# Optimization experiments

Hardware: AMD Instinct MI355X
Metric: run time of the kernel (lower is better)

Reference implementation:

```python
import jax, jax.numpy as jnp
import numpy as np

N = 100000
E = 1600000
F_IN = 128
HID = 64
N_CLASS = 40
NEG_SLOPE = 0.2


def setup_inputs() -> dict:
    key = jax.random.key(0)
    ks = jax.random.split(key, 16)
    s = lambda *sh: 1.0 / np.sqrt(sh[0])
    inp = {
        "x": jax.random.normal(ks[0], (N, F_IN), dtype=jnp.float32),
        "edge_index": jax.random.randint(ks[1], (2, E), 0, N, dtype=jnp.int64),
        "W1": jax.random.normal(ks[2], (F_IN, HID), jnp.float32) * s(F_IN),
        "b1": jnp.zeros((HID,), jnp.float32),
        "Wc0": jax.random.normal(ks[3], (HID, HID), jnp.float32) * s(HID),
        "att_src0": jax.random.normal(ks[4], (HID,), jnp.float32) * s(HID),
        "att_dst0": jax.random.normal(ks[5], (HID,), jnp.float32) * s(HID),
        "bias0": jnp.zeros((HID,), jnp.float32),
        "Wc1": jax.random.normal(ks[6], (HID, HID), jnp.float32) * s(HID),
        "att_src1": jax.random.normal(ks[7], (HID,), jnp.float32) * s(HID),
        "att_dst1": jax.random.normal(ks[8], (HID,), jnp.float32) * s(HID),
        "bias1": jnp.zeros((HID,), jnp.float32),
        "W2": jax.random.normal(ks[9], (HID, N_CLASS), jnp.float32) * s(HID),
        "b2": jnp.zeros((N_CLASS,), jnp.float32),
    }
    return inp


def gat_conv(x, src, dst, W, att_src, att_dst, bias):
    # x: [N, Fin]; src/dst: [E'] (self-loops already appended)
    h = x @ W                                   # [N, Fout]
    a_s = h @ att_src                           # [N]
    a_d = h @ att_dst                           # [N]
    e = jax.nn.leaky_relu(a_s[src] + a_d[dst], NEG_SLOPE)   # [E']
    # segment softmax over edges grouped by destination node
    e_max = jax.ops.segment_max(e, dst, num_segments=N)     # every node has a self-loop
    ex = jnp.exp(e - e_max[dst])
    denom = jax.ops.segment_sum(ex, dst, num_segments=N)
    alpha = ex / (denom[dst] + 1e-16)                        # [E']
    out = jax.ops.segment_sum(h[src] * alpha[:, None], dst, num_segments=N)
    return out + bias


def reference(x, edge_index, W1, b1, Wc0, att_src0, att_dst0, bias0,
              Wc1, att_src1, att_dst1, bias1, W2, b2):
    # eval mode: dropout_adj and feature dropout are identity
    loop = jnp.arange(N, dtype=edge_index.dtype)
    src = jnp.concatenate([edge_index[0], loop])
    dst = jnp.concatenate([edge_index[1], loop])

    h = jax.nn.relu(x @ W1 + b1)
    h = gat_conv(h, src, dst, Wc0, att_src0, att_dst0, bias0)
    h = jax.nn.relu(h)
    h = gat_conv(h, src, dst, Wc1, att_src1, att_dst1, bias1)
    logits = h @ W2 + b2
    return jax.nn.log_softmax(logits, axis=-1)
```

## Files before the change

### kernel.cpp

```cpp
#include <hip/hip_runtime.h>

#define N_NODES 100000
#define N_EDGES 1600000
#define F_IN    128
#define HID     64
#define N_CLASS 40
#define NEG_SLOPE 0.2f
#define ET (N_EDGES + N_NODES)
#define ROW_BLOCKS ((N_NODES + 63) / 64)

#define NCB   7
#define CAP1  294912
#define BPC   144
#define NFB   782
#define CAPF  2624
#define NT1   ((ET + 2047) / 2048)

typedef __attribute__((ext_vector_type(8))) short bf16x8;
typedef __attribute__((ext_vector_type(4))) float f32x4;

__device__ __forceinline__ unsigned int f2bf(float f) {
    unsigned int u = __float_as_uint(f);
    return (u + 0x7fffu + ((u >> 16) & 1u)) >> 16;
}

__global__ __launch_bounds__(256) void k_prepw(const float* __restrict__ W1,
        const float* __restrict__ Wc0, const float* __restrict__ Wc1,
        const float* __restrict__ W2,
        unsigned short* __restrict__ Wt1, unsigned short* __restrict__ Wtc0,
        unsigned short* __restrict__ Wtc1, unsigned short* __restrict__ W2t,
        int* __restrict__ zbuf, int zcount) {
    int g = blockIdx.x * 256 + threadIdx.x;
    int stride = gridDim.x * 256;
    for (int i = g; i < zcount; i += stride) zbuf[i] = 0;
    for (int i = g; i < F_IN * HID; i += stride) {
        int k = i >> 6, n = i & 63;
        Wt1[n * F_IN + k] = (unsigned short)f2bf(W1[i]);
    }
    for (int i = g; i < HID * HID; i += stride) {
        int k = i >> 6, n = i & 63;
        Wtc0[n * HID + k] = (unsigned short)f2bf(Wc0[i]);
        Wtc1[n * HID + k] = (unsigned short)f2bf(Wc1[i]);
    }
    for (int i = g; i < 48 * HID; i += stride) {
        int n = i >> 6, k = i & 63;
        W2t[n * HID + k] = (n < N_CLASS)
            ? (unsigned short)f2bf(W2[k * N_CLASS + n]) : (unsigned short)0;
    }
}

__global__ __launch_bounds__(256) void k_p1lin(
        const int* __restrict__ ei, int* __restrict__ tail1,
        unsigned int* __restrict__ buf1,
        const float* __restrict__ x, const unsigned short* __restrict__ Wt1,
        const float* __restrict__ b1, const unsigned short* __restrict__ Wtc0,
        const float* __restrict__ att_s, const float* __restrict__ att_d,
        unsigned short* __restrict__ hb, float* __restrict__ as_,
        float* __restrict__ ad_) {
    __shared__ __align__(16) char smem[17408];
    __shared__ int hist[NCB], lb[NCB], cbase[NCB];
    int t = threadIdx.x;
    int lane = t & 63, w = t >> 6;

    if (blockIdx.x < NT1) {
        unsigned int* eb = (unsigned int*)smem;
        int tileBase = blockIdx.x * 2048;
        int total = ET - tileBase; if (total > 2048) total = 2048;
        if (t < NCB) hist[t] = 0;
        __syncthreads();
        unsigned long long ltm = (1ull << lane) - 1ull;
        unsigned int pk[8]; int ps[8];
        #pragma unroll
        for (int r = 0; r < 8; ++r) {
            int i = tileBase + r * 256 + t;
            int s = 0, d = 0;
            bool valid = (i < ET);
            if (valid) {
                if (i < N_EDGES) { s = ei[i]; d = ei[N_EDGES + i]; }
                else             { s = d = i - N_EDGES; }
            }
            int b = valid ? (d >> 14) : -1;
            unsigned long long m[NCB];
            #pragma unroll
            for (int q = 0; q < NCB; ++q) m[q] = __ballot(b == q);
            int cnt = 0;
            #pragma unroll
            for (int q = 0; q < NCB; ++q) if (lane == q) cnt = __popcll(m[q]);
            int old = 0;
            if (lane < NCB) old = atomicAdd(&hist[lane], cnt);
            int bsafe = valid ? b : 0;
            int basew = __shfl(old, bsafe, 64);
            if (valid) {
                int rank = 0;
                #pragma unroll
                for (int q = 0; q < NCB; ++q)
                    if (b == q) rank = (int)__popcll(m[q] & ltm);
                pk[r] = ((unsigned int)s << 14) | ((unsigned int)d & 16383u);
                ps[r] = (basew + rank) | (b << 12);
            } else ps[r] = -1;
        }
        __syncthreads();
        if (t == 0) {
            int run = 0;
            #pragma unroll
            for (int q = 0; q < NCB; ++q) { int h = hist[q]; lb[q] = run; run += h; }
        }
        __syncthreads();
        if (t < NCB) {
            int g = (hist[t] > 0) ? atomicAdd(&tail1[t], hist[t]) : 0;
            cbase[t] = g - lb[t];
        }
        #pragma unroll
        for (int r = 0; r < 8; ++r) {
            if (ps[r] >= 0) {
                int b = ps[r] >> 12, pos = ps[r] & 4095;
                eb[lb[b] + pos] = pk[r];
            }
        }
        __syncthreads();
        int B1 = lb[1], B2 = lb[2], B3 = lb[3], B4 = lb[4], B5 = lb[5], B6 = lb[6];
        for (int j = t; j < total; j += 256) {
            unsigned int p = eb[j];
            int b = (j >= B1) + (j >= B2) + (j >= B3) + (j >= B4)
                  + (j >= B5) + (j >= B6);
            buf1[(size_t)b * CAP1 + cbase[b] + j] = p;
        }
    } else {
        int quad = lane >> 4, lr = lane & 15;
        int rowg0 = (int)(blockIdx.x - NT1) * 64 + w * 16;
        float* xs = (float*)smem + w * (16 * 68);

        int arow = rowg0 + lr; if (arow >= N_NODES) arow = N_NODES - 1;
        const float* ab = x + (size_t)arow * F_IN + quad * 8;
        float4 xa[8];
        #pragma unroll
        for (int kc = 0; kc < 4; ++kc) {
            xa[2 * kc]     = *(const float4*)(ab + kc * 32);
            xa[2 * kc + 1] = *(const float4*)(ab + kc * 32 + 4);
        }
        f32x4 zero = {0.f, 0.f, 0.f, 0.f};
        f32x4 acc[4] = {zero, zero, zero, zero};
        #pragma unroll
        for (int kc = 0; kc < 4; ++kc) {
            bf16x8 bw[4];
            #pragma unroll
            for (int nt = 0; nt < 4; ++nt)
                bw[nt] = *(const bf16x8*)(Wt1 + (nt * 16 + lr) * F_IN
                                          + kc * 32 + quad * 8);
            float4 a0 = xa[2 * kc], a1 = xa[2 * kc + 1];
            union { bf16x8 v; unsigned int u[4]; } af;
            af.u[0] = f2bf(a0.x) | (f2bf(a0.y) << 16);
            af.u[1] = f2bf(a0.z) | (f2bf(a0.w) << 16);
            af.u[2] = f2bf(a1.x) | (f2bf(a1.y) << 16);
            af.u[3] = f2bf(a1.z) | (f2bf(a1.w) << 16);
            #pragma unroll
            for (int nt = 0; nt < 4; ++nt)
                acc[nt] = __builtin_amdgcn_mfma_f32_16x16x32_bf16(
                              af.v, bw[nt], acc[nt], 0, 0, 0);
        }
        #pragma unroll
        for (int nt = 0; nt < 4; ++nt) {
            float bv = b1[nt * 16 + lr];
            #pragma unroll
            for (int reg = 0; reg < 4; ++reg)
                xs[(quad * 4 + reg) * 68 + nt * 16 + lr] =
                    fmaxf(acc[nt][reg] + bv, 0.f);
        }
        f32x4 acc2[4] = {zero, zero, zero, zero};
        #pragma unroll
        for (int kc = 0; kc < 2; ++kc) {
            bf16x8 bw[4];
            #pragma unroll
            for (int nt = 0; nt < 4; ++nt)
                bw[nt] = *(const bf16x8*)(Wtc0 + (nt * 16 + lr) * HID
                                          + kc * 32 + quad * 8);
            const float* ap = xs + lr * 68 + kc * 32 + quad * 8;
            float4 a0 = *(const float4*)ap;
            float4 a1 = *(const float4*)(ap + 4);
            union { bf16x8 v; unsigned int u[4]; } af;
            af.u[0] = f2bf(a0.x) | (f2bf(a0.y) << 16);
            af.u[1] = f2bf(a0.z) | (f2bf(a0.w) << 16);
            af.u[2] = f2bf(a1.x) | (f2bf(a1.y) << 16);
            af.u[3] = f2bf(a1.z) | (f2bf(a1.w) << 16);
            #pragma unroll
            for (int nt = 0; nt < 4; ++nt)
                acc2[nt] = __builtin_amdgcn_mfma_f32_16x16x32_bf16(
                              af.v, bw[nt], acc2[nt], 0, 0, 0);
        }
        float asv[4], adv[4];
        #pragma unroll
        for (int nt = 0; nt < 4; ++nt) {
            asv[nt] = att_s[nt * 16 + lr];
            adv[nt] = att_d[nt * 16 + lr];
        }
        #pragma unroll
        for (int reg = 0; reg < 4; ++reg) {
            float p1 = acc2[0][reg] * asv[0] + acc2[1][reg] * asv[1]
                     + acc2[2][reg] * asv[2] + acc2[3][reg] * asv[3];
            float p2 = acc2[0][reg] * adv[0] + acc2[1][reg] * adv[1]
                     + acc2[2][reg] * adv[2] + acc2[3][reg] * adv[3];
            #pragma unroll
            for (int off = 1; off < 16; off <<= 1) {
                p1 += __shfl_xor(p1, off, 64);
                p2 += __shfl_xor(p2, off, 64);
            }
            if (lr == 0) {
                int grow = rowg0 + quad * 4 + reg;
                if (grow < N_NODES) { as_[grow] = p1; ad_[grow] = p2; }
            }
        }
        #pragma unroll
        for (int nt = 0; nt < 4; ++nt)
            #pragma unroll
            for (int reg = 0; reg < 4; ++reg)
                xs[(quad * 4 + reg) * 68 + nt * 16 + lr] = acc2[nt][reg];
        #pragma unroll
        for (int j = 0; j < 2; ++j) {
            int task = j * 64 + lane;
            int r = task >> 3, g = task & 7;
            int grow = rowg0 + r;
            if (grow < N_NODES) {
                const float* p = xs + r * 68 + g * 8;
                uint4 u;
                u.x = f2bf(p[0]) | (f2bf(p[1]) << 16);
                u.y = f2bf(p[2]) | (f2bf(p[3]) << 16);
                u.z = f2bf(p[4]) | (f2bf(p[5]) << 16);
                u.w = f2bf(p[6]) | (f2bf(p[7]) << 16);
                *(uint4*)(hb + (size_t)grow * HID + g * 8) = u;
            }
        }
    }
}

__global__ __launch_bounds__(256) void k_part2(const unsigned int* __restrict__ buf1,
        const int* __restrict__ tail1, int* __restrict__ fcnt,
        unsigned int* __restrict__ buf2, int* __restrict__ fbase,
        int* __restrict__ rowptr, int* __restrict__ done0) {
    __shared__ unsigned int eb[2048];
    __shared__ int hist[128], lbase[128], loff[128], goff[128], sc[128];
    __shared__ int lastflag, wsum4[4];
    int t = threadIdx.x;
    int cb   = blockIdx.x / BPC;
    int tile = blockIdx.x % BPC;
    int n1 = tail1[cb];
    int base = tile * 2048;
    if (base < n1) {
        int total = n1 - base; if (total > 2048) total = 2048;
        if (t < 128) hist[t] = 0;
        __syncthreads();
        unsigned int pr[8]; int fr[8];
        #pragma unroll
        for (int r = 0; r < 8; ++r) {
            int i = base + r * 256 + t;
            int f = -1; unsigned int p = 0;
            if (i < n1) {
                p = buf1[(size_t)cb * CAP1 + i];
                f = (int)((p >> 7) & 127u);
                atomicAdd(&hist[f], 1);
            }
            pr[r] = p; fr[r] = f;
        }
        __syncthreads();
        if (t < 128) sc[t] = hist[t];
        __syncthreads();
        for (int off = 1; off < 128; off <<= 1) {
            int u = (t < 128 && t >= off) ? sc[t - off] : 0;
            __syncthreads();
            if (t < 128) sc[t] += u;
            __syncthreads();
        }
        if (t < 128) { lbase[t] = sc[t] - hist[t]; loff[t] = 0; }
        __syncthreads();
        if (t < 128 && hist[t] > 0)
            goff[t] = atomicAdd(&fcnt[cb * 128 + t], hist[t]);
        #pragma unroll
        for (int r = 0; r < 8; ++r) {
            if (fr[r] >= 0) {
                int f = fr[r];
                int pos = lbase[f] + atomicAdd(&loff[f], 1);
                eb[pos] = (pr[r] & 127u) | ((pr[r] >> 14) << 7)
                        | ((unsigned int)f << 24);
            }
        }
        __syncthreads();
        for (int j = t; j < total; j += 256) {
            unsigned int q = eb[j];
            int f = (int)(q >> 24);
            buf2[(size_t)(cb * 128 + f) * CAPF + goff[f] + (j - lbase[f])] =
                q & 0xFFFFFFu;
        }
    }
    if (t == 0) lastflag = (atomicAdd(done0, 1) == NCB * BPC - 1);
    __syncthreads();
    if (lastflag) {
        __threadfence();
        int k0 = t * 4;
        int v0 = (k0     < NFB) ? fcnt[k0]     : 0;
        int v1 = (k0 + 1 < NFB) ? fcnt[k0 + 1] : 0;
        int v2 = (k0 + 2 < NFB) ? fcnt[k0 + 2] : 0;
        int v3 = (k0 + 3 < NFB) ? fcnt[k0 + 3] : 0;
        int s1 = v0 + v1, s2 = s1 + v2, s3 = s2 + v3;
        int lane = t & 63, w = t >> 6;
        int ws = s3;
        #pragma unroll
        for (int off = 1; off < 64; off <<= 1) {
            int u = __shfl_up(ws, off, 64);
            if (lane >= off) ws += u;
        }
        if (lane == 63) wsum4[w] = ws;
        __syncthreads();
        int wb = 0;
        #pragma unroll
        for (int q = 0; q < 4; ++q) if (q < w) wb += wsum4[q];
        int ex = wb + ws - s3;
        if (k0     < NFB) fbase[k0]     = ex;
        if (k0 + 1 < NFB) fbase[k0 + 1] = ex + v0;
        if (k0 + 2 < NFB) fbase[k0 + 2] = ex + s1;
        if (k0 + 3 < NFB) fbase[k0 + 3] = ex + s2;
        if (t == 0) rowptr[N_NODES] = ET;
    }
}

__global__ __launch_bounds__(256) void k_part3(const unsigned int* __restrict__ buf2,
        const int* __restrict__ fcnt, const int* __restrict__ fbase,
        int* __restrict__ rowptr, int* __restrict__ col,
        int* __restrict__ dhistg, int* __restrict__ dbase,
        int* __restrict__ done1) {
    __shared__ unsigned int eb[CAPF];
    __shared__ int cs[CAPF];
    __shared__ int hist[128], lbase[128], loff[128], sc[128], dh[64];
    __shared__ int lastflag;
    int t = threadIdx.x;
    int fb = blockIdx.x;
    int nF = fcnt[fb];
    int gb = fbase[fb];
    int nbase = fb * 128;
    if (t < 128) hist[t] = 0;
    if (t >= 128 && t < 192) dh[t - 128] = 0;
    __syncthreads();
    for (int j = t; j < nF; j += 256) {
        unsigned int q = buf2[(size_t)fb * CAPF + j];
        eb[j] = q;
        atomicAdd(&hist[q & 127u], 1);
    }
    __syncthreads();
    if (t < 128) sc[t] = hist[t];
    __syncthreads();
    for (int off = 1; off < 128; off <<= 1) {
        int u = (t < 128 && t >= off) ? sc[t - off] : 0;
        __syncthreads();
        if (t < 128) sc[t] += u;
        __syncthreads();
    }
    if (t < 128) { lbase[t] = sc[t] - hist[t]; loff[t] = 0; }
    __syncthreads();
    if (t < 128 && nbase + t < N_NODES) {
        rowptr[nbase + t] = gb + lbase[t];
        int dg = hist[t]; if (dg > 63) dg = 63;
        atomicAdd(&dh[dg], 1);
    }
    for (int j = t; j < nF; j += 256) {
        unsigned int q = eb[j];
        int r = (int)(q & 127u);
        int p = lbase[r] + atomicAdd(&loff[r], 1);
        cs[p] = (int)(q >> 7);
    }
    __syncthreads();
    for (int j = t; j < nF; j += 256) col[gb + j] = cs[j];
    if (t < 64 && dh[t] > 0) atomicAdd(&dhistg[t], dh[t]);
    __syncthreads();
    if (t == 0) lastflag = (atomicAdd(done1, 1) == NFB - 1);
    __syncthreads();
    if (lastflag && t < 64) {
        __threadfence();
        int v = dhistg[t];
        int s = v;
        #pragma unroll
        for (int off = 1; off < 64; off <<= 1) {
            int u = __shfl_up(s, off, 64);
            if (t >= off) s += u;
        }
        dbase[t] = s - v;
    }
}

__global__ __launch_bounds__(256) void k_dscatter(const int* __restrict__ rowptr,
        int* __restrict__ dbase, int* __restrict__ nodeord) {
    __shared__ int lh[64], goff[64];
    int t = threadIdx.x;
    if (t < 64) lh[t] = 0;
    __syncthreads();
    int i = blockIdx.x * 256 + t;
    int deg = -1, lrank = 0;
    if (i < N_NODES) {
        deg = rowptr[i + 1] - rowptr[i];
        if (deg > 63) deg = 63;
        lrank = atomicAdd(&lh[deg], 1);
    }
    __syncthreads();
    if (t < 64) goff[t] = (lh[t] > 0) ? atomicAdd(&dbase[t], lh[t]) : 0;
    __syncthreads();
    if (deg >= 0) nodeord[goff[deg] + lrank] = i;
}

__global__ __launch_bounds__(256) void k_gemm_att(
        const unsigned short* __restrict__ hin,
        const unsigned short* __restrict__ Wt,
        const float* __restrict__ att_s, const float* __restrict__ att_d,
        unsigned short* __restrict__ hb, float* __restrict__ as_,
        float* __restrict__ ad_) {
    __shared__ float xs[4][16 * 68];
    int t = threadIdx.x;
    int lane = t & 63, w = t >> 6;
    int quad = lane >> 4, lr = lane & 15;
    int rowg0 = blockIdx.x * 64 + w * 16;

    bf16x8 bfr[2][4];
    #pragma unroll
    for (int kc = 0; kc < 2; ++kc)
        #pragma unroll
        for (int nt = 0; nt < 4; ++nt)
            bfr[kc][nt] = *(const bf16x8*)(Wt + (nt * 16 + lr) * HID
                                           + kc * 32 + quad * 8);
    f32x4 zero = {0.f, 0.f, 0.f, 0.f};
    f32x4 acc[4] = {zero, zero, zero, zero};

    int arow = rowg0 + lr; if (arow >= N_NODES) arow = N_NODES - 1;
    #pragma unroll
    for (int kc = 0; kc < 2; ++kc) {
        bf16x8 af = *(const bf16x8*)(hin + (size_t)arow * HID
                                     + kc * 32 + quad * 8);
        #pragma unroll
        for (int nt = 0; nt < 4; ++nt)
            acc[nt] = __builtin_amdgcn_mfma_f32_16x16x32_bf16(
                          af, bfr[kc][nt], acc[nt], 0, 0, 0);
    }
    float asv[4], adv[4];
    #pragma unroll
    for (int nt = 0; nt < 4; ++nt) {
        asv[nt] = att_s[nt * 16 + lr];
        adv[nt] = att_d[nt * 16 + lr];
    }
    #pragma unroll
    for (int reg = 0; reg < 4; ++reg) {
        float p1 = acc[0][reg] * asv[0] + acc[1][reg] * asv[1]
                 + acc[2][reg] * asv[2] + acc[3][reg] * asv[3];
        float p2 = acc[0][reg] * adv[0] + acc[1][reg] * adv[1]
                 + acc[2][reg] * adv[2] + acc[3][reg] * adv[3];
        #pragma unroll
        for (int off = 1; off < 16; off <<= 1) {
            p1 += __shfl_xor(p1, off, 64);
            p2 += __shfl_xor(p2, off, 64);
        }
        if (lr == 0) {
            int grow = rowg0 + quad * 4 + reg;
            if (grow < N_NODES) { as_[grow] = p1; ad_[grow] = p2; }
        }
    }
    #pragma unroll
    for (int nt = 0; nt < 4; ++nt)
        #pragma unroll
        for (int reg = 0; reg < 4; ++reg)
            xs[w][(quad * 4 + reg) * 68 + nt * 16 + lr] = acc[nt][reg];
    #pragma unroll
    for (int j = 0; j < 2; ++j) {
        int task = j * 64 + lane;
        int r = task >> 3, g = task & 7;
        int grow = rowg0 + r;
        if (grow < N_NODES) {
            const float* p = xs[w] + r * 68 + g * 8;
            uint4 u;
            u.x = f2bf(p[0]) | (f2bf(p[1]) << 16);
            u.y = f2bf(p[2]) | (f2bf(p[3]) << 16);
            u.z = f2bf(p[4]) | (f2bf(p[5]) << 16);
            u.w = f2bf(p[6]) | (f2bf(p[7]) << 16);
            *(uint4*)(hb + (size_t)grow * HID + g * 8) = u;
        }
    }
}

template <bool RELU>
__global__ __launch_bounds__(256) void k_gat_agg(const int* __restrict__ rowptr,
        const int* __restrict__ col, const unsigned short* __restrict__ hb,
        const float* __restrict__ as_, const float* __restrict__ ad_,
        const float* __restrict__ bias, const int* __restrict__ nodeord,
        unsigned short* __restrict__ outb) {
    int t = threadIdx.x;
    int lane = t & 63;
    int wid = blockIdx.x * 4 + (t >> 6);
    int l8 = lane & 7;
    int ch = l8 * 8;
    int d = nodeord[wid * 8 + (lane >> 3)];
    int beg = rowptr[d];
    int deg = rowptr[d + 1] - beg;
    float add = ad_[d];
    int degw = deg;
    degw = max(degw, __shfl_xor(degw, 8, 64));
    degw = max(degw, __shfl_xor(degw, 16, 64));
    degw = max(degw, __shfl_xor(degw, 32, 64));

    float a0=0.f,a1=0.f,a2=0.f,a3=0.f,a4=0.f,a5=0.f,a6=0.f,a7=0.f,den=0.f;
    const unsigned short* hch = hb + ch;
    for (int c = 0; c < degw; c += 8) {
        int idx = c + l8;
        int sj = 0; float wj = 0.f;
        if (idx < deg) {
            sj = col[beg + idx];
            float e = as_[sj] + add;
            e = (e > 0.f) ? e : NEG_SLOPE * e;
            wj = __expf(e);
        }
        uint4 hv[8]; float w0[8];
        #pragma unroll
        for (int j = 0; j < 8; ++j) {
            int sl = (lane & 56) | j;
            int s = __shfl(sj, sl, 64);
            w0[j] = __shfl(wj, sl, 64);
            hv[j] = *(const uint4*)(hch + (size_t)s * HID);
        }
        #pragma unroll
        for (int j = 0; j < 8; ++j) {
            den += w0[j];
            a0 = fmaf(w0[j], __uint_as_float(hv[j].x << 16),         a0);
            a1 = fmaf(w0[j], __uint_as_float(hv[j].x & 0xffff0000u), a1);
            a2 = fmaf(w0[j], __uint_as_float(hv[j].y << 16),         a2);
            a3 = fmaf(w0[j], __uint_as_float(hv[j].y & 0xffff0000u), a3);
            a4 = fmaf(w0[j], __uint_as_float(hv[j].z << 16),         a4);
            a5 = fmaf(w0[j], __uint_as_float(hv[j].z & 0xffff0000u), a5);
            a6 = fmaf(w0[j], __uint_as_float(hv[j].w << 16),         a6);
            a7 = fmaf(w0[j], __uint_as_float(hv[j].w & 0xffff0000u), a7);
        }
    }
    float inv = 1.f / (den + 1e-16f);
    float4 bA = *(const float4*)(bias + ch);
    float4 bB = *(const float4*)(bias + ch + 4);
    float o0 = fmaf(a0, inv, bA.x), o1 = fmaf(a1, inv, bA.y);
    float o2 = fmaf(a2, inv, bA.z), o3 = fmaf(a3, inv, bA.w);
    float o4 = fmaf(a4, inv, bB.x), o5 = fmaf(a5, inv, bB.y);
    float o6 = fmaf(a6, inv, bB.z), o7 = fmaf(a7, inv, bB.w);
    if (RELU) {
        o0 = fmaxf(o0, 0.f); o1 = fmaxf(o1, 0.f);
        o2 = fmaxf(o2, 0.f); o3 = fmaxf(o3, 0.f);
        o4 = fmaxf(o4, 0.f); o5 = fmaxf(o5, 0.f);
        o6 = fmaxf(o6, 0.f); o7 = fmaxf(o7, 0.f);
    }
    uint4 u;
    u.x = f2bf(o0) | (f2bf(o1) << 16);
    u.y = f2bf(o2) | (f2bf(o3) << 16);
    u.z = f2bf(o4) | (f2bf(o5) << 16);
    u.w = f2bf(o6) | (f2bf(o7) << 16);
    *(uint4*)(outb + (size_t)d * HID + ch) = u;
}

__global__ __launch_bounds__(256) void k_final(
        const unsigned short* __restrict__ aggb,
        const unsigned short* __restrict__ W2t, const float* __restrict__ b2,
        float* __restrict__ out) {
    __shared__ float xs[64 * 44];
    int t = threadIdx.x;
    int lane = t & 63, w = t >> 6;
    int quad = lane >> 4, lr = lane & 15;
    int rowg0 = blockIdx.x * 64 + w * 16;
    int base = blockIdx.x * 64;
    int rem = N_NODES - base; if (rem > 64) rem = 64;

    bf16x8 bfr[2][3];
    #pragma unroll
    for (int kc = 0; kc < 2; ++kc)
        #pragma unroll
        for (int nt = 0; nt < 3; ++nt)
            bfr[kc][nt] = *(const bf16x8*)(W2t + (nt * 16 + lr) * HID
                                           + kc * 32 + quad * 8);
    f32x4 zero = {0.f, 0.f, 0.f, 0.f};
    f32x4 acc[3] = {zero, zero, zero};
    int arow = rowg0 + lr; if (arow >= N_NODES) arow = N_NODES - 1;
    #pragma unroll
    for (int kc = 0; kc < 2; ++kc) {
        bf16x8 af = *(const bf16x8*)(aggb + (size_t)arow * HID
                                     + kc * 32 + quad * 8);
        #pragma unroll
        for (int nt = 0; nt < 3; ++nt)
            acc[nt] = __builtin_amdgcn_mfma_f32_16x16x32_bf16(
                          af, bfr[kc][nt], acc[nt], 0, 0, 0);
    }
    float bc[3];
    #pragma unroll
    for (int nt = 0; nt < 3; ++nt) {
        int cl = nt * 16 + lr;
        bc[nt] = (cl < N_CLASS) ? b2[cl] : -1e30f;
    }
    #pragma unroll
    for (int reg = 0; reg < 4; ++reg) {
        float v0 = acc[0][reg] + bc[0];
        float v1 = acc[1][reg] + bc[1];
        float v2 = acc[2][reg] + bc[2];
        float m = fmaxf(fmaxf(v0, v1), v2);
        #pragma unroll
        for (int off = 1; off < 16; off <<= 1)
            m = fmaxf(m, __shfl_xor(m, off, 64));
        float ss = __expf(v0 - m) + __expf(v1 - m) + __expf(v2 - m);
        #pragma unroll
        for (int off = 1; off < 16; off <<= 1)
            ss += __shfl_xor(ss, off, 64);
        float lse = m + logf(ss);
        int r = w * 16 + quad * 4 + reg;
        xs[r * 44 + lr]      = v0 - lse;
        xs[r * 44 + 16 + lr] = v1 - lse;
        if (lr < 8) xs[r * 44 + 32 + lr] = v2 - lse;
    }
    __syncthreads();
    #pragma unroll
    for (int j = 0; j < 3; ++j) {
        int idx = j * 256 + t;
        if (idx < rem * 10) {
            int r = idx / 10, c4 = idx - r * 10;
            float4 v = *(const float4*)(xs + r * 44 + c4 * 4);
            *(float4*)(out + (size_t)base * N_CLASS + idx * 4) = v;
        }
    }
}

extern "C" void kernel_launch(void* const* d_in, const int* in_sizes, int n_in,
                              void* d_out, int out_size, void* d_ws, size_t ws_size,
                              hipStream_t stream) {
    const float* x     = (const float*)d_in[0];
    const int*   ei    = (const int*)  d_in[1];
    const float* W1    = (const float*)d_in[2];
    const float* b1    = (const float*)d_in[3];
    const float* Wc0   = (const float*)d_in[4];
    const float* as0   = (const float*)d_in[5];
    const float* ad0   = (const float*)d_in[6];
    const float* bias0 = (const float*)d_in[7];
    const float* Wc1   = (const float*)d_in[8];
    const float* as1   = (const float*)d_in[9];
    const float* ad1   = (const float*)d_in[10];
    const float* bias1 = (const float*)d_in[11];
    const float* W2    = (const float*)d_in[12];
    const float* b2    = (const float*)d_in[13];
    float* out = (float*)d_out;

    char* p = (char*)d_ws;
    unsigned short* hb    = (unsigned short*)p; p += (size_t)N_NODES * HID * 2;
    unsigned short* agg0b = (unsigned short*)p; p += (size_t)N_NODES * HID * 2;
    char* pbuf = p;
    unsigned int*   buf1  = (unsigned int*)pbuf;
    unsigned int*   buf2  = (unsigned int*)(pbuf + (size_t)NCB * CAP1 * 4);
    unsigned short* agg1b = (unsigned short*)pbuf;
    p += (size_t)NCB * CAP1 * 4 + (size_t)NFB * CAPF * 4;
    int* col = (int*)p;                          p += (size_t)ET * 4;
    unsigned short* Wt1  = (unsigned short*)p;   p += F_IN * HID * 2;
    unsigned short* Wtc0 = (unsigned short*)p;   p += HID * HID * 2;
    unsigned short* Wtc1 = (unsigned short*)p;   p += HID * HID * 2;
    unsigned short* W2t  = (unsigned short*)p;   p += 48 * HID * 2;
    float* as_ = (float*)p;                      p += (size_t)N_NODES * 4;
    float* ad_ = (float*)p;                      p += (size_t)N_NODES * 4;
    int* tail1 = (int*)p;
    int* fcnt  = tail1 + NCB;
    int* fbase = fcnt + NFB;
    int* dhist = fbase + NFB;
    int* dbase = dhist + 64;
    int* done  = dbase + 64;
    const int ZCOUNT = NCB + 2 * NFB + 128 + 2;
    p += (size_t)ZCOUNT * 4;
    int* rowptr  = (int*)p;                      p += (size_t)(N_NODES + 1) * 4;
    int* nodeord = (int*)p;

    const int AGG_BLOCKS  = N_NODES / 32;
    const int NODE_BLOCKS = (N_NODES + 255) / 256;

    k_prepw<<<32, 256, 0, stream>>>(W1, Wc0, Wc1, W2, Wt1, Wtc0, Wtc1, W2t,
                                    tail1, ZCOUNT);
    k_p1lin<<<NT1 + ROW_BLOCKS, 256, 0, stream>>>(
        ei, tail1, buf1, x, Wt1, b1, Wtc0, as0, ad0, hb, as_, ad_);
    k_part2<<<NCB * BPC, 256, 0, stream>>>(buf1, tail1, fcnt, buf2, fbase,
                                           rowptr, done + 0);
    k_part3<<<NFB, 256, 0, stream>>>(buf2, fcnt, fbase, rowptr, col, dhist,
                                     dbase, done + 1);
    k_dscatter<<<NODE_BLOCKS, 256, 0, stream>>>(rowptr, dbase, nodeord);

    k_gat_agg<true><<<AGG_BLOCKS, 256, 0, stream>>>(
        rowptr, col, hb, as_, ad_, bias0, nodeord, agg0b);

    k_gemm_att<<<ROW_BLOCKS, 256, 0, stream>>>(agg0b, Wtc1, as1, ad1,
                                               hb, as_, ad_);
    k_gat_agg<false><<<AGG_BLOCKS, 256, 0, stream>>>(
        rowptr, col, hb, as_, ad_, bias1, nodeord, agg1b);

    k_final<<<ROW_BLOCKS, 256, 0, stream>>>(agg1b, W2t, b2, out);
}
```

Before: 289.9 us.

## Fuse next-layer linear and final classifier into GAT aggregation kernels

Removes the separate gemm_att and final classifier kernels. Each node's aggregated row is staged in LDS and multiplied by Wc1 (layer 0) or W2 with log-softmax (layer 1) inside the aggregation kernel, using fp32 FMAs instead of MFMA. It also software-pipelines the col/attention-weight fetch one chunk ahead in the aggregation loop and pads the degree histogram counters to separate cache lines. This saves two launches and a round trip of intermediates through memory, at the cost of scalar per-lane GEMM work, global weight reads in the inner loop, and uncoalesced 5-float output stores.

```diff
diff --git a/kernel.cpp b/kernel.cpp
--- a/kernel.cpp
+++ b/kernel.cpp
@@ -25,10 +25,8 @@
 }
 
 __global__ __launch_bounds__(256) void k_prepw(const float* __restrict__ W1,
-        const float* __restrict__ Wc0, const float* __restrict__ Wc1,
-        const float* __restrict__ W2,
+        const float* __restrict__ Wc0,
         unsigned short* __restrict__ Wt1, unsigned short* __restrict__ Wtc0,
-        unsigned short* __restrict__ Wtc1, unsigned short* __restrict__ W2t,
         int* __restrict__ zbuf, int zcount) {
     int g = blockIdx.x * 256 + threadIdx.x;
     int stride = gridDim.x * 256;
@@ -40,12 +38,6 @@
     for (int i = g; i < HID * HID; i += stride) {
         int k = i >> 6, n = i & 63;
         Wtc0[n * HID + k] = (unsigned short)f2bf(Wc0[i]);
-        Wtc1[n * HID + k] = (unsigned short)f2bf(Wc1[i]);
-    }
-    for (int i = g; i < 48 * HID; i += stride) {
-        int n = i >> 6, k = i & 63;
-        W2t[n * HID + k] = (n < N_CLASS)
-            ? (unsigned short)f2bf(W2[k * N_CLASS + n]) : (unsigned short)0;
     }
 }
 
@@ -367,20 +359,20 @@
     }
     __syncthreads();
     for (int j = t; j < nF; j += 256) col[gb + j] = cs[j];
-    if (t < 64 && dh[t] > 0) atomicAdd(&dhistg[t], dh[t]);
+    if (t < 64 && dh[t] > 0) atomicAdd(&dhistg[t * 16], dh[t]);
     __syncthreads();
     if (t == 0) lastflag = (atomicAdd(done1, 1) == NFB - 1);
     __syncthreads();
     if (lastflag && t < 64) {
         __threadfence();
-        int v = dhistg[t];
+        int v = dhistg[t * 16];
         int s = v;
         #pragma unroll
         for (int off = 1; off < 64; off <<= 1) {
             int u = __shfl_up(s, off, 64);
             if (t >= off) s += u;
         }
-        dbase[t] = s - v;
+        dbase[t * 16] = s - v;
     }
 }
 
@@ -398,99 +390,31 @@
         lrank = atomicAdd(&lh[deg], 1);
     }
     __syncthreads();
-    if (t < 64) goff[t] = (lh[t] > 0) ? atomicAdd(&dbase[t], lh[t]) : 0;
+    if (t < 64) goff[t] = (lh[t] > 0) ? atomicAdd(&dbase[t * 16], lh[t]) : 0;
     __syncthreads();
     if (deg >= 0) nodeord[goff[deg] + lrank] = i;
 }
 
-__global__ __launch_bounds__(256) void k_gemm_att(
-        const unsigned short* __restrict__ hin,
-        const unsigned short* __restrict__ Wt,
-        const float* __restrict__ att_s, const float* __restrict__ att_d,
-        unsigned short* __restrict__ hb, float* __restrict__ as_,
-        float* __restrict__ ad_) {
-    __shared__ float xs[4][16 * 68];
-    int t = threadIdx.x;
-    int lane = t & 63, w = t >> 6;
-    int quad = lane >> 4, lr = lane & 15;
-    int rowg0 = blockIdx.x * 64 + w * 16;
-
-    bf16x8 bfr[2][4];
-    #pragma unroll
-    for (int kc = 0; kc < 2; ++kc)
-        #pragma unroll
-        for (int nt = 0; nt < 4; ++nt)
-            bfr[kc][nt] = *(const bf16x8*)(Wt + (nt * 16 + lr) * HID
-                                           + kc * 32 + quad * 8);
-    f32x4 zero = {0.f, 0.f, 0.f, 0.f};
-    f32x4 acc[4] = {zero, zero, zero, zero};
-
-    int arow = rowg0 + lr; if (arow >= N_NODES) arow = N_NODES - 1;
-    #pragma unroll
-    for (int kc = 0; kc < 2; ++kc) {
-        bf16x8 af = *(const bf16x8*)(hin + (size_t)arow * HID
-                                     + kc * 32 + quad * 8);
-        #pragma unroll
-        for (int nt = 0; nt < 4; ++nt)
-            acc[nt] = __builtin_amdgcn_mfma_f32_16x16x32_bf16(
-                          af, bfr[kc][nt], acc[nt], 0, 0, 0);
-    }
-    float asv[4], adv[4];
-    #pragma unroll
-    for (int nt = 0; nt < 4; ++nt) {
-        asv[nt] = att_s[nt * 16 + lr];
-        adv[nt] = att_d[nt * 16 + lr];
-    }
-    #pragma unroll
-    for (int reg = 0; reg < 4; ++reg) {
-        float p1 = acc[0][reg] * asv[0] + acc[1][reg] * asv[1]
-                 + acc[2][reg] * asv[2] + acc[3][reg] * asv[3];
-        float p2 = acc[0][reg] * adv[0] + acc[1][reg] * adv[1]
-                 + acc[2][reg] * adv[2] + acc[3][reg] * adv[3];
-        #pragma unroll
-        for (int off = 1; off < 16; off <<= 1) {
-            p1 += __shfl_xor(p1, off, 64);
-            p2 += __shfl_xor(p2, off, 64);
-        }
-        if (lr == 0) {
-            int grow = rowg0 + quad * 4 + reg;
-            if (grow < N_NODES) { as_[grow] = p1; ad_[grow] = p2; }
-        }
-    }
-    #pragma unroll
-    for (int nt = 0; nt < 4; ++nt)
-        #pragma unroll
-        for (int reg = 0; reg < 4; ++reg)
-            xs[w][(quad * 4 + reg) * 68 + nt * 16 + lr] = acc[nt][reg];
-    #pragma unroll
-    for (int j = 0; j < 2; ++j) {
-        int task = j * 64 + lane;
-        int r = task >> 3, g = task & 7;
-        int grow = rowg0 + r;
-        if (grow < N_NODES) {
-            const float* p = xs[w] + r * 68 + g * 8;
-            uint4 u;
-            u.x = f2bf(p[0]) | (f2bf(p[1]) << 16);
-            u.y = f2bf(p[2]) | (f2bf(p[3]) << 16);
-            u.z = f2bf(p[4]) | (f2bf(p[5]) << 16);
-            u.w = f2bf(p[6]) | (f2bf(p[7]) << 16);
-            *(uint4*)(hb + (size_t)grow * HID + g * 8) = u;
-        }
-    }
-}
-
-template <bool RELU>
-__global__ __launch_bounds__(256) void k_gat_agg(const int* __restrict__ rowptr,
-        const int* __restrict__ col, const unsigned short* __restrict__ hb,
+template <int LAYER>
+__global__ __launch_bounds__(256) void k_agg(const int* __restrict__ rowptr,
+        const int* __restrict__ col, const unsigned short* __restrict__ hin,
         const float* __restrict__ as_, const float* __restrict__ ad_,
         const float* __restrict__ bias, const int* __restrict__ nodeord,
-        unsigned short* __restrict__ outb) {
+        const float* __restrict__ Wn,
+        const float* __restrict__ attS, const float* __restrict__ attD,
+        const float* __restrict__ b2,
+        unsigned short* __restrict__ hout,
+        float* __restrict__ aso, float* __restrict__ ado,
+        float* __restrict__ out) {
+    __shared__ float rows[4][8][68];
     int t = threadIdx.x;
     int lane = t & 63;
-    int wid = blockIdx.x * 4 + (t >> 6);
+    int w = t >> 6;
+    int wid = blockIdx.x * 4 + w;
     int l8 = lane & 7;
+    int g = lane >> 3;
     int ch = l8 * 8;
-    int d = nodeord[wid * 8 + (lane >> 3)];
+    int d = nodeord[wid * 8 + g];
     int beg = rowptr[d];
     int deg = rowptr[d + 1] - beg;
     float add = ad_[d];
@@ -500,16 +424,16 @@
     degw = max(degw, __shfl_xor(degw, 32, 64));
 
     float a0=0.f,a1=0.f,a2=0.f,a3=0.f,a4=0.f,a5=0.f,a6=0.f,a7=0.f,den=0.f;
-    const unsigned short* hch = hb + ch;
+    const unsigned short* hch = hin + ch;
+
+    int sj = 0; float wj = 0.f;
+    if (l8 < deg) {
+        sj = col[beg + l8];
+        float e = as_[sj] + add;
+        e = (e > 0.f) ? e : NEG_SLOPE * e;
+        wj = __expf(e);
+    }
     for (int c = 0; c < degw; c += 8) {
-        int idx = c + l8;
-        int sj = 0; float wj = 0.f;
-        if (idx < deg) {
-            sj = col[beg + idx];
-            float e = as_[sj] + add;
-            e = (e > 0.f) ? e : NEG_SLOPE * e;
-            wj = __expf(e);
-        }
         uint4 hv[8]; float w0[8];
         #pragma unroll
         for (int j = 0; j < 8; ++j) {
@@ -518,6 +442,15 @@
             w0[j] = __shfl(wj, sl, 64);
             hv[j] = *(const uint4*)(hch + (size_t)s * HID);
         }
+        int sjn = 0; float wjn = 0.f;
+        int idxn = c + 8 + l8;
+        if (c + 8 < degw && idxn < deg) {
+            sjn = col[beg + idxn];
+            float e = as_[sjn] + add;
+            e = (e > 0.f) ? e : NEG_SLOPE * e;
+            wjn = __expf(e);
+        }
+        __builtin_amdgcn_sched_barrier(0);
         #pragma unroll
         for (int j = 0; j < 8; ++j) {
             den += w0[j];
@@ -530,6 +463,7 @@
             a6 = fmaf(w0[j], __uint_as_float(hv[j].w << 16),         a6);
             a7 = fmaf(w0[j], __uint_as_float(hv[j].w & 0xffff0000u), a7);
         }
+        sj = sjn; wj = wjn;
     }
     float inv = 1.f / (den + 1e-16f);
     float4 bA = *(const float4*)(bias + ch);
@@ -538,85 +472,84 @@
     float o2 = fmaf(a2, inv, bA.z), o3 = fmaf(a3, inv, bA.w);
     float o4 = fmaf(a4, inv, bB.x), o5 = fmaf(a5, inv, bB.y);
     float o6 = fmaf(a6, inv, bB.z), o7 = fmaf(a7, inv, bB.w);
-    if (RELU) {
+    if (LAYER == 0) {
         o0 = fmaxf(o0, 0.f); o1 = fmaxf(o1, 0.f);
         o2 = fmaxf(o2, 0.f); o3 = fmaxf(o3, 0.f);
         o4 = fmaxf(o4, 0.f); o5 = fmaxf(o5, 0.f);
         o6 = fmaxf(o6, 0.f); o7 = fmaxf(o7, 0.f);
     }
-    uint4 u;
-    u.x = f2bf(o0) | (f2bf(o1) << 16);
-    u.y = f2bf(o2) | (f2bf(o3) << 16);
-    u.z = f2bf(o4) | (f2bf(o5) << 16);
-    u.w = f2bf(o6) | (f2bf(o7) << 16);
-    *(uint4*)(outb + (size_t)d * HID + ch) = u;
-}
-
-__global__ __launch_bounds__(256) void k_final(
-        const unsigned short* __restrict__ aggb,
-        const unsigned short* __restrict__ W2t, const float* __restrict__ b2,
-        float* __restrict__ out) {
-    __shared__ float xs[64 * 44];
-    int t = threadIdx.x;
-    int lane = t & 63, w = t >> 6;
-    int quad = lane >> 4, lr = lane & 15;
-    int rowg0 = blockIdx.x * 64 + w * 16;
-    int base = blockIdx.x * 64;
-    int rem = N_NODES - base; if (rem > 64) rem = 64;
-
-    bf16x8 bfr[2][3];
-    #pragma unroll
-    for (int kc = 0; kc < 2; ++kc)
-        #pragma unroll
-        for (int nt = 0; nt < 3; ++nt)
-            bfr[kc][nt] = *(const bf16x8*)(W2t + (nt * 16 + lr) * HID
-                                           + kc * 32 + quad * 8);
-    f32x4 zero = {0.f, 0.f, 0.f, 0.f};
-    f32x4 acc[3] = {zero, zero, zero};
-    int arow = rowg0 + lr; if (arow >= N_NODES) arow = N_NODES - 1;
-    #pragma unroll
-    for (int kc = 0; kc < 2; ++kc) {
-        bf16x8 af = *(const bf16x8*)(aggb + (size_t)arow * HID
-                                     + kc * 32 + quad * 8);
-        #pragma unroll
-        for (int nt = 0; nt < 3; ++nt)
-            acc[nt] = __builtin_amdgcn_mfma_f32_16x16x32_bf16(
-                          af, bfr[kc][nt], acc[nt], 0, 0, 0);
-    }
-    float bc[3];
-    #pragma unroll
-    for (int nt = 0; nt < 3; ++nt) {
-        int cl = nt * 16 + lr;
-        bc[nt] = (cl < N_CLASS) ? b2[cl] : -1e30f;
-    }
-    #pragma unroll
-    for (int reg = 0; reg < 4; ++reg) {
-        float v0 = acc[0][reg] + bc[0];
-        float v1 = acc[1][reg] + bc[1];
-        float v2 = acc[2][reg] + bc[2];
-        float m = fmaxf(fmaxf(v0, v1), v2);
-        #pragma unroll
-        for (int off = 1; off < 16; off <<= 1)
-            m = fmaxf(m, __shfl_xor(m, off, 64));
-        float ss = __expf(v0 - m) + __expf(v1 - m) + __expf(v2 - m);
-        #pragma unroll
-        for (int off = 1; off < 16; off <<= 1)
-            ss += __shfl_xor(ss, off, 64);
+
+    float* myrow = &rows[w][g][0];
+    myrow[ch + 0] = o0; myrow[ch + 1] = o1; myrow[ch + 2] = o2;
+    myrow[ch + 3] = o3; myrow[ch + 4] = o4; myrow[ch + 5] = o5;
+    myrow[ch + 6] = o6; myrow[ch + 7] = o7;
+
+    if (LAYER == 0) {
+        float h1[8] = {0,0,0,0,0,0,0,0};
+        for (int k = 0; k < 64; k += 4) {
+            float4 rv = *(const float4*)(myrow + k);
+            #pragma unroll
+            for (int kk = 0; kk < 4; ++kk) {
+                float r = (kk == 0) ? rv.x : (kk == 1) ? rv.y
+                        : (kk == 2) ? rv.z : rv.w;
+                float4 wa = *(const float4*)(Wn + (k + kk) * 64 + ch);
+                float4 wb = *(const float4*)(Wn + (k + kk) * 64 + ch + 4);
+                h1[0] = fmaf(r, wa.x, h1[0]); h1[1] = fmaf(r, wa.y, h1[1]);
+                h1[2] = fmaf(r, wa.z, h1[2]); h1[3] = fmaf(r, wa.w, h1[3]);
+                h1[4] = fmaf(r, wb.x, h1[4]); h1[5] = fmaf(r, wb.y, h1[5]);
+                h1[6] = fmaf(r, wb.z, h1[6]); h1[7] = fmaf(r, wb.w, h1[7]);
+            }
+        }
+        float4 sA = *(const float4*)(attS + ch);
+        float4 sB = *(const float4*)(attS + ch + 4);
+        float4 dA = *(const float4*)(attD + ch);
+        float4 dB = *(const float4*)(attD + ch + 4);
+        float p1 = h1[0]*sA.x + h1[1]*sA.y + h1[2]*sA.z + h1[3]*sA.w
+                 + h1[4]*sB.x + h1[5]*sB.y + h1[6]*sB.z + h1[7]*sB.w;
+        float p2 = h1[0]*dA.x + h1[1]*dA.y + h1[2]*dA.z + h1[3]*dA.w
+                 + h1[4]*dB.x + h1[5]*dB.y + h1[6]*dB.z + h1[7]*dB.w;
+        p1 += __shfl_xor(p1, 1, 64); p1 += __shfl_xor(p1, 2, 64);
+        p1 += __shfl_xor(p1, 4, 64);
+        p2 += __shfl_xor(p2, 1, 64); p2 += __shfl_xor(p2, 2, 64);
+        p2 += __shfl_xor(p2, 4, 64);
+        if (l8 == 0) { aso[d] = p1; ado[d] = p2; }
+        uint4 u;
+        u.x = f2bf(h1[0]) | (f2bf(h1[1]) << 16);
+        u.y = f2bf(h1[2]) | (f2bf(h1[3]) << 16);
+        u.z = f2bf(h1[4]) | (f2bf(h1[5]) << 16);
+        u.w = f2bf(h1[6]) | (f2bf(h1[7]) << 16);
+        *(uint4*)(hout + (size_t)d * HID + ch) = u;
+    } else {
+        int nb = l8 * 5;
+        float lg[5];
+        #pragma unroll
+        for (int c = 0; c < 5; ++c) lg[c] = b2[nb + c];
+        for (int k = 0; k < 64; k += 4) {
+            float4 rv = *(const float4*)(myrow + k);
+            #pragma unroll
+            for (int kk = 0; kk < 4; ++kk) {
+                float r = (kk == 0) ? rv.x : (kk == 1) ? rv.y
+                        : (kk == 2) ? rv.z : rv.w;
+                const float* wr = Wn + (k + kk) * N_CLASS + nb;
+                lg[0] = fmaf(r, wr[0], lg[0]);
+                lg[1] = fmaf(r, wr[1], lg[1]);
+                lg[2] = fmaf(r, wr[2], lg[2]);
+                lg[3] = fmaf(r, wr[3], lg[3]);
+                lg[4] = fmaf(r, wr[4], lg[4]);
+            }
+        }
+        float m = fmaxf(fmaxf(fmaxf(lg[0], lg[1]), fmaxf(lg[2], lg[3])), lg[4]);
+        m = fmaxf(m, __shfl_xor(m, 1, 64));
+        m = fmaxf(m, __shfl_xor(m, 2, 64));
+        m = fmaxf(m, __shfl_xor(m, 4, 64));
+        float ss = __expf(lg[0]-m) + __expf(lg[1]-m) + __expf(lg[2]-m)
+                 + __expf(lg[3]-m) + __expf(lg[4]-m);
+        ss += __shfl_xor(ss, 1, 64); ss += __shfl_xor(ss, 2, 64);
+        ss += __shfl_xor(ss, 4, 64);
         float lse = m + logf(ss);
-        int r = w * 16 + quad * 4 + reg;
-        xs[r * 44 + lr]      = v0 - lse;
-        xs[r * 44 + 16 + lr] = v1 - lse;
-        if (lr < 8) xs[r * 44 + 32 + lr] = v2 - lse;
-    }
-    __syncthreads();
-    #pragma unroll
-    for (int j = 0; j < 3; ++j) {
-        int idx = j * 256 + t;
-        if (idx < rem * 10) {
-            int r = idx / 10, c4 = idx - r * 10;
-            float4 v = *(const float4*)(xs + r * 44 + c4 * 4);
-            *(float4*)(out + (size_t)base * N_CLASS + idx * 4) = v;
-        }
+        float* op = out + (size_t)d * N_CLASS + nb;
+        op[0] = lg[0] - lse; op[1] = lg[1] - lse; op[2] = lg[2] - lse;
+        op[3] = lg[3] - lse; op[4] = lg[4] - lse;
     }
 }
 
@@ -640,51 +573,44 @@
     float* out = (float*)d_out;
 
     char* p = (char*)d_ws;
-    unsigned short* hb    = (unsigned short*)p; p += (size_t)N_NODES * HID * 2;
-    unsigned short* agg0b = (unsigned short*)p; p += (size_t)N_NODES * HID * 2;
-    char* pbuf = p;
-    unsigned int*   buf1  = (unsigned int*)pbuf;
-    unsigned int*   buf2  = (unsigned int*)(pbuf + (size_t)NCB * CAP1 * 4);
-    unsigned short* agg1b = (unsigned short*)pbuf;
-    p += (size_t)NCB * CAP1 * 4 + (size_t)NFB * CAPF * 4;
-    int* col = (int*)p;                          p += (size_t)ET * 4;
-    unsigned short* Wt1  = (unsigned short*)p;   p += F_IN * HID * 2;
-    unsigned short* Wtc0 = (unsigned short*)p;   p += HID * HID * 2;
-    unsigned short* Wtc1 = (unsigned short*)p;   p += HID * HID * 2;
-    unsigned short* W2t  = (unsigned short*)p;   p += 48 * HID * 2;
-    float* as_ = (float*)p;                      p += (size_t)N_NODES * 4;
-    float* ad_ = (float*)p;                      p += (size_t)N_NODES * 4;
+    unsigned short* hb   = (unsigned short*)p; p += (size_t)N_NODES * HID * 2;
+    unsigned short* hb2  = (unsigned short*)p; p += (size_t)N_NODES * HID * 2;
+    unsigned int*   buf1 = (unsigned int*)p;   p += (size_t)NCB * CAP1 * 4;
+    unsigned int*   buf2 = (unsigned int*)p;   p += (size_t)NFB * CAPF * 4;
+    int* col = (int*)p;                        p += (size_t)ET * 4;
+    unsigned short* Wt1  = (unsigned short*)p; p += F_IN * HID * 2;
+    unsigned short* Wtc0 = (unsigned short*)p; p += HID * HID * 2;
+    float* as0_ = (float*)p;                   p += (size_t)N_NODES * 4;
+    float* ad0_ = (float*)p;                   p += (size_t)N_NODES * 4;
+    float* as1_ = (float*)p;                   p += (size_t)N_NODES * 4;
+    float* ad1_ = (float*)p;                   p += (size_t)N_NODES * 4;
     int* tail1 = (int*)p;
     int* fcnt  = tail1 + NCB;
     int* fbase = fcnt + NFB;
     int* dhist = fbase + NFB;
-    int* dbase = dhist + 64;
-    int* done  = dbase + 64;
-    const int ZCOUNT = NCB + 2 * NFB + 128 + 2;
+    int* dbase = dhist + 64 * 16;
+    int* done  = dbase + 64 * 16;
+    const int ZCOUNT = NCB + 2 * NFB + 2 * 64 * 16 + 2;
     p += (size_t)ZCOUNT * 4;
-    int* rowptr  = (int*)p;                      p += (size_t)(N_NODES + 1) * 4;
+    int* rowptr  = (int*)p;                    p += (size_t)(N_NODES + 1) * 4;
     int* nodeord = (int*)p;
 
     const int AGG_BLOCKS  = N_NODES / 32;
     const int NODE_BLOCKS = (N_NODES + 255) / 256;
 
-    k_prepw<<<32, 256, 0, stream>>>(W1, Wc0, Wc1, W2, Wt1, Wtc0, Wtc1, W2t,
-                                    tail1, ZCOUNT);
+    k_prepw<<<32, 256, 0, stream>>>(W1, Wc0, Wt1, Wtc0, tail1, ZCOUNT);
     k_p1lin<<<NT1 + ROW_BLOCKS, 256, 0, stream>>>(
-        ei, tail1, buf1, x, Wt1, b1, Wtc0, as0, ad0, hb, as_, ad_);
+        ei, tail1, buf1, x, Wt1, b1, Wtc0, as0, ad0, hb, as0_, ad0_);
     k_part2<<<NCB * BPC, 256, 0, stream>>>(buf1, tail1, fcnt, buf2, fbase,
                                            rowptr, done + 0);
     k_part3<<<NFB, 256, 0, stream>>>(buf2, fcnt, fbase, rowptr, col, dhist,
                                      dbase, done + 1);
     k_dscatter<<<NODE_BLOCKS, 256, 0, stream>>>(rowptr, dbase, nodeord);
 
-    k_gat_agg<true><<<AGG_BLOCKS, 256, 0, stream>>>(
-        rowptr, col, hb, as_, ad_, bias0, nodeord, agg0b);
-
-    k_gemm_att<<<ROW_BLOCKS, 256, 0, stream>>>(agg0b, Wtc1, as1, ad1,
-                                               hb, as_, ad_);
-    k_gat_agg<false><<<AGG_BLOCKS, 256, 0, stream>>>(
-        rowptr, col, hb, as_, ad_, bias1, nodeord, agg1b);
-
-    k_final<<<ROW_BLOCKS, 256, 0, stream>>>(agg1b, W2t, b2, out);
-}
+    k_agg<0><<<AGG_BLOCKS, 256, 0, stream>>>(
+        rowptr, col, hb, as0_, ad0_, bias0, nodeord,
+        Wc1, as1, ad1, nullptr, hb2, as1_, ad1_, nullptr);
+    k_agg<1><<<AGG_BLOCKS, 256, 0, stream>>>(
+        rowptr, col, hb2, as1_, ad1_, bias1, nodeord,
+        W2, nullptr, nullptr, b2, nullptr, nullptr, nullptr, out);
+}
```

Result: slower. 335.6 us (+15.8%).
